# Kernel optimization log

Hardware: AMD Instinct MI355X
Metric: run time of the kernel (lower is better)

Reference implementation:

```python
import jax, jax.numpy as jnp
import numpy as np

# decoded layout constants
NN, NO, SD = 16, 8, 4          # num_neighbors, num_obstacles, state_dim_per_agent
B = 131072                      # batch rows
H1, E, HP, AD = 64, 16, 64, 2   # phi hidden, embed, psi hidden, action dim
D_ROBOT, D_OBST = 0.3, 0.3
B_GAMMA, B_EXPH = 0.05, 1.0
PHI_MIN, PHI_MAX = -2.0, 2.0
A_MAX = 2.0


def setup_inputs() -> dict:
    key = jax.random.key(0)
    kx, kw = jax.random.split(key)
    # x: [count | goal(SD) | NN neighbor rel-states (SD each) | NO obstacle rel-pos (2 each)]
    x = jax.random.normal(kx, (B, 1 + SD + SD * NN + 2 * NO), dtype=jnp.float32) * 2.0
    x = x.at[:, 0].set(float(NN))
    names = [("Wp1n", (SD, H1)), ("bp1n", (H1,)), ("Wp2n", (H1, E)), ("bp2n", (E,)),
             ("Wr1n", (E, H1)), ("br1n", (H1,)), ("Wr2n", (H1, E)), ("br2n", (E,)),
             ("Wp1o", (2, H1)), ("bp1o", (H1,)), ("Wp2o", (H1, E)), ("bp2o", (E,)),
             ("Wr1o", (E, H1)), ("br1o", (H1,)), ("Wr2o", (H1, E)), ("br2o", (E,)),
             ("Wpsi1", (2 * E + SD, HP)), ("bpsi1", (HP,)), ("Wpsi2", (HP, AD)), ("bpsi2", (AD,))]
    ks = jax.random.split(kw, len(names))
    inp = {"x": x}
    for (n, sh), k in zip(names, ks):
        s = 1.0 / np.sqrt(sh[0])  # torch Linear default init scale
        inp[n] = jax.random.uniform(k, sh, jnp.float32, -s, s)
    return inp


def _mlp2(h, W1, b1, W2, b2):
    # Feedforward: activation between layers, linear output
    return jax.nn.relu(h @ W1 + b1) @ W2 + b2


def _deepset(el, Wp1, bp1, Wp2, bp2, Wr1, br1, Wr2, br2):
    # el: [B, n, d] -> phi each element, sum over set, rho
    phi = _mlp2(el, Wp1, bp1, Wp2, bp2)          # [B, n, E]
    return _mlp2(phi.sum(axis=1), Wr1, br1, Wr2, br2)  # [B, E]


def _barrier_sum(P, D):
    # P: [B, n, 2]; APF barrier gamma * P / (|P| * (|P|-D)^exph), summed over n
    nrm = jnp.linalg.norm(P, axis=-1, keepdims=True)   # [B, n, 1]
    H = nrm - D
    return (B_GAMMA * P / (nrm * H ** B_EXPH)).sum(axis=1)  # [B, 2]


def reference(x, Wp1n, bp1n, Wp2n, bp2n, Wr1n, br1n, Wr2n, br2n,
              Wp1o, bp1o, Wp2o, bp2o, Wr1o, br1o, Wr2o, br2o,
              Wpsi1, bpsi1, Wpsi2, bpsi2):
    nb = x.shape[0]
    g = x[:, 1:1 + SD]                                        # goal
    nbr = x[:, 1 + SD:1 + SD + SD * NN].reshape(nb, NN, SD)   # neighbor rel-states
    obs = x[:, 1 + SD + SD * NN:].reshape(nb, NO, 2)          # obstacle rel-pos

    rho_n = _deepset(nbr, Wp1n, bp1n, Wp2n, bp2n, Wr1n, br1n, Wr2n, br2n)
    rho_o = _deepset(obs, Wp1o, bp1o, Wp2o, bp2o, Wr1o, br1o, Wr2o, br2o)

    h = jnp.concatenate([rho_n, rho_o, g], axis=1)            # [B, 2E+SD]
    emp = _mlp2(h, Wpsi1, bpsi1, Wpsi2, bpsi2)                # psi network
    emp = (jnp.tanh(emp) + 1.0) / 2.0 * (PHI_MAX - PHI_MIN) + PHI_MIN  # scale_empty

    bar = _barrier_sum(-nbr[:, :, :2], D_ROBOT) + _barrier_sum(-obs, D_OBST)

    action = emp + bar
    # scale(): divide rows whose inf-norm exceeds a_max
    inv_alpha = jnp.maximum(jnp.max(jnp.abs(action), axis=1, keepdims=True) / A_MAX, 1.0)
    return action / inv_alpha
```

## Files before the change

kernel.cpp:

```cpp
#include <hip/hip_runtime.h>
#include <math.h>


typedef __attribute__((ext_vector_type(8))) _Float16 f16x8;
typedef __attribute__((ext_vector_type(2))) __fp16 fp16x2;
typedef __attribute__((ext_vector_type(4))) float f32x4;

#define XW 85

#define FR_S1N  0
#define FR_S1O  4
#define FR_G2N  8
#define FR_G2O  10
#define FR_RNA  12
#define FR_RNB  16
#define FR_ROA  18
#define FR_ROB  22
#define FR_PSI1 24
#define FR_PSI2 32
#define N_FRAGS 34

#define BIG_STR 144
#define PHI_STR 80
#define CAT_STR 144
#define L_BIGN 0
#define L_BIGO 2304
#define L_PHN  4608
#define L_PHO  5888
#define L_CAT  7168
#define L_OUT  9472
#define L_BAR  9600
#define GRP_LDS 9728
#define NBA_STR 136
#define OBA_STR 68

#define H16_ONE 0x00003C00u

__device__ __forceinline__ float fast_rcp(float x)  { return __builtin_amdgcn_rcpf(x); }
__device__ __forceinline__ float fast_sqrt(float x) { return __builtin_amdgcn_sqrtf(x); }

__device__ __forceinline__ float two_tanh(float a) {
    float ax = fabsf(a);
    float e = __expf(2.0f * ax);
    float t = 1.0f - 2.0f * fast_rcp(e + 1.0f);
    return copysignf(2.0f * t, a);
}

__device__ __forceinline__ void lds_order() {
    __asm__ __volatile__("" ::: "memory");
}

__device__ __forceinline__ unsigned pk2(float a, float b) {
    union { fp16x2 h; unsigned u; } t;
    t.h = __builtin_amdgcn_cvt_pkrtz(a, b);
    return t.u;
}
__device__ __forceinline__ f16x8 lds_af(const char* area, int stride, int off, int lane) {
    int mm = lane & 15, qq = lane >> 4;
    return *(const f16x8*)(area + mm * stride + off + qq * 16);
}
__device__ __forceinline__ f16x8 load_bh(const _Float16* wsf, int frag, int lane) {
    return ((const f16x8*)(wsf + (size_t)frag * 512))[lane];
}
__device__ __forceinline__ f32x4 cinit(float b) {
    f32x4 c; c[0] = b; c[1] = b; c[2] = b; c[3] = b; return c;
}
__device__ __forceinline__ f32x4 mfma1(f16x8 a, f16x8 b, f32x4 c) {
    return __builtin_amdgcn_mfma_f32_16x16x32_f16(a, b, c, 0, 0, 0);
}

__global__ void bn_prep(const float* __restrict__ Wp1n, const float* __restrict__ Wp2n,
                        const float* __restrict__ Wr1n, const float* __restrict__ Wr2n,
                        const float* __restrict__ Wp1o, const float* __restrict__ Wp2o,
                        const float* __restrict__ Wr1o, const float* __restrict__ Wr2o,
                        const float* __restrict__ Wpsi1, const float* __restrict__ Wpsi2,
                        const float* __restrict__ bp1n, const float* __restrict__ bp1o,
                        const float* __restrict__ br1n, const float* __restrict__ br1o,
                        const float* __restrict__ bpsi1,
                        _Float16* __restrict__ wsf)
{
    int f = blockIdx.x;
    int lane = threadIdx.x;
    const float* W; const float* bias = nullptr;
    int K, N, kk = 0, nt = 0, rel, kbias = -1;
    if (f < 4)        { W = Wp1n;  K = 4;  N = 64; nt = f;      bias = bp1n;  kbias = 4; }
    else if (f < 8)   { W = Wp1o;  K = 2;  N = 64; nt = f - 4;  bias = bp1o;  kbias = 2; }
    else if (f < 10)  { W = Wp2n;  K = 64; N = 16; kk = f - 8; }
    else if (f < 12)  { W = Wp2o;  K = 64; N = 16; kk = f - 10; }
    else if (f < 16)  { W = Wr1n;  K = 16; N = 64; nt = f - 12; bias = br1n;  kbias = 16; }
    else if (f < 18)  { W = Wr2n;  K = 64; N = 16; kk = f - 16; }
    else if (f < 22)  { W = Wr1o;  K = 16; N = 64; nt = f - 18; bias = br1o;  kbias = 16; }
    else if (f < 24)  { W = Wr2o;  K = 64; N = 16; kk = f - 22; }
    else if (f < 32)  { rel = f - 24; W = Wpsi1; K = 36; N = 64; kk = rel >> 2; nt = rel & 3;
                        bias = bpsi1; kbias = 36; }
    else              { W = Wpsi2; K = 64; N = 2;  kk = f - 32; }

    int q = lane >> 4, c = lane & 15;
    _Float16* dst = wsf + (size_t)f * 512 + lane * 8;
    for (int j = 0; j < 8; ++j) {
        int k = kk * 32 + q * 8 + j;
        int n = nt * 16 + c;
        float v = 0.f;
        if (n < N) {
            if (k < K) v = W[k * N + n];
            else if (k == kbias) v = bias[n];
        }
        dst[j] = (_Float16)v;
    }
}

__global__ __launch_bounds__(256, 8) void bn_main(
    const float* __restrict__ x, const _Float16* __restrict__ wsf,
    const float* __restrict__ bp2n, const float* __restrict__ br2n,
    const float* __restrict__ bp2o, const float* __restrict__ br2o,
    const float* __restrict__ bpsi2,
    float* __restrict__ out, int nb)
{
    __shared__ char smem[2 * GRP_LDS];
    const int lane = threadIdx.x & 63;
    const int wid  = threadIdx.x >> 6;
    const int grp  = wid >> 1;
    const int role = wid & 1;
    const int group = blockIdx.x * 2 + grp;
    const int row0 = group * 16;

    char* Gl   = smem + grp * GRP_LDS;
    char* BIGN = Gl + L_BIGN;
    char* BIGO = Gl + L_BIGO;
    char* PHN  = Gl + L_PHN;
    char* PHO  = Gl + L_PHO;
    char* CAT  = Gl + L_CAT;
    char* OUTA = Gl + L_OUT;
    char* BAR  = Gl + L_BAR;
    char* NBA  = BIGN;
    char* OBA  = BIGO;

    const int m = lane & 15, q = lane >> 4, c = m;
    const float* xg   = x + (size_t)row0 * XW;
    const float* xrow = xg + (size_t)m * XW;

    const f32x4 ZC = cinit(0.f);

    if (role == 0) {
        {
            int ln5 = lane >> 5;
            int pr  = lane & 31;
            int mm0 = pr >> 1, fp = pr & 1;
            char* db = NBA + mm0 * NBA_STR + fp * 4;
            const float* s0 = xg + (size_t)ln5 * XW + 5 + pr * 2;
            #pragma unroll
            for (int t = 0; t < 8; ++t) {
                const float* s = s0 + (size_t)(2 * t) * XW;
                *(unsigned*)(db + (2 * t + ln5) * 8) = pk2(s[0], s[1]);
            }
        }

        {
            unsigned zv = ((lane & 7) == 0) ? H16_ONE : 0u;
            for (int i = lane; i < 128; i += 64) {
                int r = i >> 3, d = i & 7;
                *(unsigned*)(PHN + r * PHI_STR + 32 + d * 4) = zv;
            }
        }
        lds_order();

        f16x8 Bs1n[4];
        #pragma unroll
        for (int nt = 0; nt < 4; ++nt) Bs1n[nt] = load_bh(wsf, FR_S1N + nt, lane);

        {
            const int m8 = m * 8;
            f32x4 acc[4];
            #pragma unroll
            for (int nt = 0; nt < 4; ++nt) acc[nt] = cinit(0.f);
            union { f16x8 v; unsigned u[4]; uint2 h[2]; } A;
            A.u[2] = H16_ONE; A.u[3] = 0;
            #pragma unroll 8
            for (int mm = 0; mm < 16; ++mm) {
                A.h[0] = *(const uint2*)(NBA + mm * NBA_STR + m8);
                #pragma unroll
                for (int nt = 0; nt < 4; ++nt) {
                    f32x4 cc = mfma1(A.v, Bs1n[nt], ZC);
                    #pragma unroll
                    for (int reg = 0; reg < 4; ++reg)
                        acc[nt][reg] += fmaxf(cc[reg], 0.f);
                }
            }
            lds_order();
            #pragma unroll
            for (int nt = 0; nt < 4; ++nt)
                #pragma unroll
                for (int reg = 0; reg < 4; ++reg)
                    *(_Float16*)(BIGN + (q * 4 + reg) * BIG_STR + (nt * 16 + c) * 2)
                        = (_Float16)acc[nt][reg];
        }
        lds_order();

        {
            float b_g2n = 16.f * bp2n[c];
            f16x8 Bg2n0 = load_bh(wsf, FR_G2N + 0, lane);
            f16x8 Bg2n1 = load_bh(wsf, FR_G2N + 1, lane);
            f16x8 A0 = lds_af(BIGN, BIG_STR, 0, lane);
            f16x8 A1 = lds_af(BIGN, BIG_STR, 64, lane);
            f32x4 ca = mfma1(A0, Bg2n0, cinit(b_g2n));
            f32x4 cb = mfma1(A1, Bg2n1, ZC);
            #pragma unroll
            for (int reg = 0; reg < 4; ++reg)
                *(_Float16*)(PHN + (q * 4 + reg) * PHI_STR + c * 2) = (_Float16)(ca[reg] + cb[reg]);
        }
        lds_order();

        {
            f16x8 Brna[4];
            #pragma unroll
            for (int nt = 0; nt < 4; ++nt) Brna[nt] = load_bh(wsf, FR_RNA + nt, lane);
            f16x8 A = lds_af(PHN, PHI_STR, 0, lane);
            #pragma unroll
            for (int nt = 0; nt < 4; ++nt) {
                f32x4 cc = mfma1(A, Brna[nt], ZC);
                #pragma unroll
                for (int reg = 0; reg < 4; ++reg)
                    *(_Float16*)(BIGN + (q * 4 + reg) * BIG_STR + (nt * 16 + c) * 2) = (_Float16)fmaxf(cc[reg], 0.f);
            }
        }
        lds_order();

        {
            float b_rnb = br2n[c];
            f16x8 Brnb0 = load_bh(wsf, FR_RNB + 0, lane);
            f16x8 Brnb1 = load_bh(wsf, FR_RNB + 1, lane);
            f16x8 A0 = lds_af(BIGN, BIG_STR, 0, lane);
            f16x8 A1 = lds_af(BIGN, BIG_STR, 64, lane);
            f32x4 ca = mfma1(A0, Brnb0, cinit(b_rnb));
            f32x4 cb = mfma1(A1, Brnb1, ZC);
            #pragma unroll
            for (int reg = 0; reg < 4; ++reg)
                *(_Float16*)(CAT + (q * 4 + reg) * CAT_STR + c * 2) = (_Float16)(ca[reg] + cb[reg]);
        }
    } else {
        {
            int r8 = lane >> 3;
            int oo = lane & 7;
            char* db = OBA + oo * OBA_STR;
            const float* s0 = xg + (size_t)r8 * XW + 69 + oo * 2;
            #pragma unroll
            for (int t = 0; t < 2; ++t) {
                const float* s = s0 + (size_t)(8 * t) * XW;
                *(unsigned*)(db + (8 * t + r8) * 4) = pk2(s[0], s[1]);
            }
        }

        {
            unsigned zv = ((lane & 7) == 0) ? H16_ONE : 0u;
            for (int i = lane; i < 128; i += 64) {
                int r = i >> 3, d = i & 7;
                *(unsigned*)(PHO + r * PHI_STR + 32 + d * 4) = zv;
            }
        }
        {
            unsigned zc = ((lane & 15) == 2) ? H16_ONE : 0u;
            for (int i = lane; i < 256; i += 64) {
                int r = i >> 4, d = i & 15;
                *(unsigned*)(CAT + r * CAT_STR + 64 + d * 4) = zc;
            }
        }
        lds_order();

        if (lane < 16) {
            const float* xr = x + (size_t)(row0 + lane) * XW;
            uint2 gv;
            gv.x = pk2(xr[1], xr[2]);
            gv.y = pk2(xr[3], xr[4]);
            *(uint2*)(CAT + lane * CAT_STR + 64) = gv;
        }

        {
            float bx = 0.f, by = 0.f;
            #pragma unroll
            for (int i = 0; i < 4; ++i) {
                int n = 4 * q + i;
                float px = -xrow[5 + 4 * n], py = -xrow[6 + 4 * n];
                float nrm = fast_sqrt(px * px + py * py);
                float coef = 0.05f * fast_rcp(nrm * (nrm - 0.3f));
                bx = fmaf(coef, px, bx);
                by = fmaf(coef, py, by);
            }
            #pragma unroll
            for (int i = 0; i < 2; ++i) {
                int o = 2 * q + i;
                float px = -xrow[69 + 2 * o], py = -xrow[70 + 2 * o];
                float nrm = fast_sqrt(px * px + py * py);
                float coef = 0.05f * fast_rcp(nrm * (nrm - 0.3f));
                bx = fmaf(coef, px, bx);
                by = fmaf(coef, py, by);
            }
            bx += __shfl_xor(bx, 16); by += __shfl_xor(by, 16);
            bx += __shfl_xor(bx, 32); by += __shfl_xor(by, 32);
            if (q == 0) { float2 bb; bb.x = bx; bb.y = by; *(float2*)(BAR + m * 8) = bb; }
        }

        f16x8 Bs1o[4];
        #pragma unroll
        for (int nt = 0; nt < 4; ++nt) Bs1o[nt] = load_bh(wsf, FR_S1O + nt, lane);

        {
            const int m4 = m * 4;
            f32x4 acc[4];
            #pragma unroll
            for (int nt = 0; nt < 4; ++nt) acc[nt] = cinit(0.f);
            union { f16x8 v; unsigned u[4]; } A;
            A.u[1] = H16_ONE; A.u[2] = 0; A.u[3] = 0;
            #pragma unroll
            for (int oo = 0; oo < 8; ++oo) {
                A.u[0] = *(const unsigned*)(OBA + oo * OBA_STR + m4);
                #pragma unroll
                for (int nt = 0; nt < 4; ++nt) {
                    f32x4 cc = mfma1(A.v, Bs1o[nt], ZC);
                    #pragma unroll
                    for (int reg = 0; reg < 4; ++reg)
                        acc[nt][reg] += fmaxf(cc[reg], 0.f);
                }
            }
            lds_order();
            #pragma unroll
            for (int nt = 0; nt < 4; ++nt)
                #pragma unroll
                for (int reg = 0; reg < 4; ++reg)
                    *(_Float16*)(BIGO + (q * 4 + reg) * BIG_STR + (nt * 16 + c) * 2)
                        = (_Float16)acc[nt][reg];
        }
        lds_order();

        {
            float b_g2o = 8.f * bp2o[c];
            f16x8 Bg2o0 = load_bh(wsf, FR_G2O + 0, lane);
            f16x8 Bg2o1 = load_bh(wsf, FR_G2O + 1, lane);
            f16x8 A0 = lds_af(BIGO, BIG_STR, 0, lane);
            f16x8 A1 = lds_af(BIGO, BIG_STR, 64, lane);
            f32x4 ca = mfma1(A0, Bg2o0, cinit(b_g2o));
            f32x4 cb = mfma1(A1, Bg2o1, ZC);
            #pragma unroll
            for (int reg = 0; reg < 4; ++reg)
                *(_Float16*)(PHO + (q * 4 + reg) * PHI_STR + c * 2) = (_Float16)(ca[reg] + cb[reg]);
        }
        lds_order();

        {
            f16x8 Broa[4];
            #pragma unroll
            for (int nt = 0; nt < 4; ++nt) Broa[nt] = load_bh(wsf, FR_ROA + nt, lane);
            f16x8 A = lds_af(PHO, PHI_STR, 0, lane);
            #pragma unroll
            for (int nt = 0; nt < 4; ++nt) {
                f32x4 cc = mfma1(A, Broa[nt], ZC);
                #pragma unroll
                for (int reg = 0; reg < 4; ++reg)
                    *(_Float16*)(BIGO + (q * 4 + reg) * BIG_STR + (nt * 16 + c) * 2) = (_Float16)fmaxf(cc[reg], 0.f);
            }
        }
        lds_order();

        {
            float b_rob = br2o[c];
            f16x8 Brob0 = load_bh(wsf, FR_ROB + 0, lane);
            f16x8 Brob1 = load_bh(wsf, FR_ROB + 1, lane);
            f16x8 A0 = lds_af(BIGO, BIG_STR, 0, lane);
            f16x8 A1 = lds_af(BIGO, BIG_STR, 64, lane);
            f32x4 ca = mfma1(A0, Brob0, cinit(b_rob));
            f32x4 cb = mfma1(A1, Brob1, ZC);
            #pragma unroll
            for (int reg = 0; reg < 4; ++reg)
                *(_Float16*)(CAT + (q * 4 + reg) * CAT_STR + (16 + c) * 2) = (_Float16)(ca[reg] + cb[reg]);
        }
    }

    __syncthreads();

    if (role == 1) {
        f16x8 Bp1a[4], Bp1b[4], Bp2[2];
        #pragma unroll
        for (int nt = 0; nt < 4; ++nt) Bp1a[nt] = load_bh(wsf, FR_PSI1 + nt, lane);
        #pragma unroll
        for (int nt = 0; nt < 4; ++nt) Bp1b[nt] = load_bh(wsf, FR_PSI1 + 4 + nt, lane);
        Bp2[0] = load_bh(wsf, FR_PSI2 + 0, lane);
        Bp2[1] = load_bh(wsf, FR_PSI2 + 1, lane);

        {
            f16x8 A0 = lds_af(CAT, CAT_STR, 0, lane);
            f16x8 A1 = lds_af(CAT, CAT_STR, 64, lane);
            #pragma unroll
            for (int nt = 0; nt < 4; ++nt) {
                f32x4 ca = mfma1(A0, Bp1a[nt], ZC);
                f32x4 cb = mfma1(A1, Bp1b[nt], ZC);
                #pragma unroll
                for (int reg = 0; reg < 4; ++reg)
                    *(_Float16*)(BIGO + (q * 4 + reg) * BIG_STR + (nt * 16 + c) * 2) = (_Float16)fmaxf(ca[reg] + cb[reg], 0.f);
            }
        }
        lds_order();

        {
            float b_p2 = (c < 2) ? bpsi2[c] : 0.f;
            f16x8 A0 = lds_af(BIGO, BIG_STR, 0, lane);
            f16x8 A1 = lds_af(BIGO, BIG_STR, 64, lane);
            f32x4 ca = mfma1(A0, Bp2[0], cinit(b_p2));
            f32x4 cb = mfma1(A1, Bp2[1], ZC);
            if (c < 2) {
                #pragma unroll
                for (int reg = 0; reg < 4; ++reg)
                    *(float*)(OUTA + (q * 4 + reg) * 8 + c * 4) = ca[reg] + cb[reg];
            }
        }
        lds_order();

        if (lane < 16) {
            float2 a  = *(const float2*)(OUTA + lane * 8);
            float2 bb = *(const float2*)(BAR + lane * 8);
            float a0 = two_tanh(a.x) + bb.x;
            float a1 = two_tanh(a.y) + bb.y;
            float amax = fmaxf(fabsf(a0), fabsf(a1));
            float inv_alpha = fmaxf(amax * 0.5f, 1.0f);
            float rr = fast_rcp(inv_alpha);
            float2 o; o.x = a0 * rr; o.y = a1 * rr;
            *(float2*)(out + (size_t)(row0 + lane) * 2) = o;
        }
    }
}

extern "C" void kernel_launch(void* const* d_in, const int* in_sizes, int n_in,
                              void* d_out, int out_size, void* d_ws, size_t ws_size,
                              hipStream_t stream) {
    const float* x     = (const float*)d_in[0];
    const float* Wp1n  = (const float*)d_in[1];
    const float* bp1n  = (const float*)d_in[2];
    const float* Wp2n  = (const float*)d_in[3];
    const float* bp2n  = (const float*)d_in[4];
    const float* Wr1n  = (const float*)d_in[5];
    const float* br1n  = (const float*)d_in[6];
    const float* Wr2n  = (const float*)d_in[7];
    const float* br2n  = (const float*)d_in[8];
    const float* Wp1o  = (const float*)d_in[9];
    const float* bp1o  = (const float*)d_in[10];
    const float* Wp2o  = (const float*)d_in[11];
    const float* bp2o  = (const float*)d_in[12];
    const float* Wr1o  = (const float*)d_in[13];
    const float* br1o  = (const float*)d_in[14];
    const float* Wr2o  = (const float*)d_in[15];
    const float* br2o  = (const float*)d_in[16];
    const float* Wpsi1 = (const float*)d_in[17];
    const float* bpsi1 = (const float*)d_in[18];
    const float* Wpsi2 = (const float*)d_in[19];
    const float* bpsi2 = (const float*)d_in[20];
    float* out = (float*)d_out;

    int nb = in_sizes[0] / XW;
    _Float16* wsf = (_Float16*)d_ws;

    bn_prep<<<N_FRAGS, 64, 0, stream>>>(Wp1n, Wp2n, Wr1n, Wr2n,
                                        Wp1o, Wp2o, Wr1o, Wr2o,
                                        Wpsi1, Wpsi2,
                                        bp1n, bp1o, br1n, br1o, bpsi1,
                                        wsf);

    int groups = (nb + 15) / 16;
    int blocks = (groups + 1) / 2;
    bn_main<<<blocks, 256, 0, stream>>>(x, wsf,
                                        bp2n, br2n, bp2o, br2o, bpsi2,
                                        out, nb);
}
```

Before: 145.4 us.

## Process each 16-row group with one wavefront instead of two cooperating waves

Before, two waves shared each 16-row group: one ran the neighbor deep-set, the other the obstacle deep-set, barrier and psi, joined by a block-wide barrier. Now each wave handles a whole group serially with a smaller, reused per-wave LDS region, so a 256-thread block covers four groups and the __syncthreads disappears. The aim is to drop the cross-wave sync and shrink LDS per group. The cost is a longer serial dependency chain per wave and less overlap between the two branches. Launch bounds drop from 8 to 6 blocks per CU.

```diff
diff --git a/kernel.cpp b/kernel.cpp
--- a/kernel.cpp
+++ b/kernel.cpp
@@ -23,14 +23,13 @@
 #define BIG_STR 144
 #define PHI_STR 80
 #define CAT_STR 144
-#define L_BIGN 0
-#define L_BIGO 2304
-#define L_PHN  4608
-#define L_PHO  5888
-#define L_CAT  7168
-#define L_OUT  9472
-#define L_BAR  9600
-#define GRP_LDS 9728
+#define L_BIG  0
+#define L_PHI  2304
+#define L_CAT  3584
+#define L_OUT  5888
+#define L_BAR  6016
+#define L_OBA  6144
+#define GRP_LDS 6688
 #define NBA_STR 136
 #define OBA_STR 68
 
@@ -109,31 +108,27 @@
     }
 }
 
-__global__ __launch_bounds__(256, 8) void bn_main(
+__global__ __launch_bounds__(256, 6) void bn_main(
     const float* __restrict__ x, const _Float16* __restrict__ wsf,
     const float* __restrict__ bp2n, const float* __restrict__ br2n,
     const float* __restrict__ bp2o, const float* __restrict__ br2o,
     const float* __restrict__ bpsi2,
     float* __restrict__ out, int nb)
 {
-    __shared__ char smem[2 * GRP_LDS];
+    __shared__ char smem[4 * GRP_LDS];
     const int lane = threadIdx.x & 63;
     const int wid  = threadIdx.x >> 6;
-    const int grp  = wid >> 1;
-    const int role = wid & 1;
-    const int group = blockIdx.x * 2 + grp;
+    const int group = blockIdx.x * 4 + wid;
     const int row0 = group * 16;
 
-    char* Gl   = smem + grp * GRP_LDS;
-    char* BIGN = Gl + L_BIGN;
-    char* BIGO = Gl + L_BIGO;
-    char* PHN  = Gl + L_PHN;
-    char* PHO  = Gl + L_PHO;
+    char* Gl   = smem + wid * GRP_LDS;
+    char* BIG  = Gl + L_BIG;
+    char* PHI  = Gl + L_PHI;
     char* CAT  = Gl + L_CAT;
     char* OUTA = Gl + L_OUT;
     char* BAR  = Gl + L_BAR;
-    char* NBA  = BIGN;
-    char* OBA  = BIGO;
+    char* OBA  = Gl + L_OBA;
+    char* NBA  = BIG;
 
     const int m = lane & 15, q = lane >> 4, c = m;
     const float* xg   = x + (size_t)row0 * XW;
@@ -141,289 +136,273 @@
 
     const f32x4 ZC = cinit(0.f);
 
-    if (role == 0) {
-        {
-            int ln5 = lane >> 5;
-            int pr  = lane & 31;
-            int mm0 = pr >> 1, fp = pr & 1;
-            char* db = NBA + mm0 * NBA_STR + fp * 4;
-            const float* s0 = xg + (size_t)ln5 * XW + 5 + pr * 2;
-            #pragma unroll
-            for (int t = 0; t < 8; ++t) {
-                const float* s = s0 + (size_t)(2 * t) * XW;
-                *(unsigned*)(db + (2 * t + ln5) * 8) = pk2(s[0], s[1]);
-            }
-        }
-
-        {
-            unsigned zv = ((lane & 7) == 0) ? H16_ONE : 0u;
-            for (int i = lane; i < 128; i += 64) {
-                int r = i >> 3, d = i & 7;
-                *(unsigned*)(PHN + r * PHI_STR + 32 + d * 4) = zv;
-            }
-        }
-        lds_order();
-
+    {
+        int ln5 = lane >> 5;
+        int pr  = lane & 31;
+        int mm0 = pr >> 1, fp = pr & 1;
+        char* db = NBA + mm0 * NBA_STR + fp * 4;
+        const float* s0 = xg + (size_t)ln5 * XW + 5 + pr * 2;
+        #pragma unroll
+        for (int t = 0; t < 8; ++t) {
+            const float* s = s0 + (size_t)(2 * t) * XW;
+            *(unsigned*)(db + (2 * t + ln5) * 8) = pk2(s[0], s[1]);
+        }
+    }
+    {
+        int r8 = lane >> 3;
+        int oo = lane & 7;
+        char* db = OBA + oo * OBA_STR;
+        const float* s0 = xg + (size_t)r8 * XW + 69 + oo * 2;
+        #pragma unroll
+        for (int t = 0; t < 2; ++t) {
+            const float* s = s0 + (size_t)(8 * t) * XW;
+            *(unsigned*)(db + (8 * t + r8) * 4) = pk2(s[0], s[1]);
+        }
+    }
+
+    {
+        unsigned zv = ((lane & 7) == 0) ? H16_ONE : 0u;
+        for (int i = lane; i < 128; i += 64) {
+            int r = i >> 3, d = i & 7;
+            *(unsigned*)(PHI + r * PHI_STR + 32 + d * 4) = zv;
+        }
+    }
+    {
+        unsigned zc = ((lane & 15) == 2) ? H16_ONE : 0u;
+        for (int i = lane; i < 256; i += 64) {
+            int r = i >> 4, d = i & 15;
+            *(unsigned*)(CAT + r * CAT_STR + 64 + d * 4) = zc;
+        }
+    }
+    if (lane < 16) {
+        const float* xr = x + (size_t)(row0 + lane) * XW;
+        uint2 gv;
+        gv.x = pk2(xr[1], xr[2]);
+        gv.y = pk2(xr[3], xr[4]);
+        *(uint2*)(CAT + lane * CAT_STR + 64) = gv;
+    }
+
+    {
+        float bx = 0.f, by = 0.f;
+        #pragma unroll
+        for (int i = 0; i < 4; ++i) {
+            int n = 4 * q + i;
+            float px = -xrow[5 + 4 * n], py = -xrow[6 + 4 * n];
+            float nrm = fast_sqrt(px * px + py * py);
+            float coef = 0.05f * fast_rcp(nrm * (nrm - 0.3f));
+            bx = fmaf(coef, px, bx);
+            by = fmaf(coef, py, by);
+        }
+        #pragma unroll
+        for (int i = 0; i < 2; ++i) {
+            int o = 2 * q + i;
+            float px = -xrow[69 + 2 * o], py = -xrow[70 + 2 * o];
+            float nrm = fast_sqrt(px * px + py * py);
+            float coef = 0.05f * fast_rcp(nrm * (nrm - 0.3f));
+            bx = fmaf(coef, px, bx);
+            by = fmaf(coef, py, by);
+        }
+        bx += __shfl_xor(bx, 16); by += __shfl_xor(by, 16);
+        bx += __shfl_xor(bx, 32); by += __shfl_xor(by, 32);
+        if (q == 0) { float2 bb; bb.x = bx; bb.y = by; *(float2*)(BAR + m * 8) = bb; }
+    }
+    lds_order();
+
+    {
         f16x8 Bs1n[4];
         #pragma unroll
         for (int nt = 0; nt < 4; ++nt) Bs1n[nt] = load_bh(wsf, FR_S1N + nt, lane);
 
-        {
-            const int m8 = m * 8;
-            f32x4 acc[4];
-            #pragma unroll
-            for (int nt = 0; nt < 4; ++nt) acc[nt] = cinit(0.f);
-            union { f16x8 v; unsigned u[4]; uint2 h[2]; } A;
-            A.u[2] = H16_ONE; A.u[3] = 0;
-            #pragma unroll 8
-            for (int mm = 0; mm < 16; ++mm) {
-                A.h[0] = *(const uint2*)(NBA + mm * NBA_STR + m8);
-                #pragma unroll
-                for (int nt = 0; nt < 4; ++nt) {
-                    f32x4 cc = mfma1(A.v, Bs1n[nt], ZC);
-                    #pragma unroll
-                    for (int reg = 0; reg < 4; ++reg)
-                        acc[nt][reg] += fmaxf(cc[reg], 0.f);
-                }
-            }
-            lds_order();
-            #pragma unroll
-            for (int nt = 0; nt < 4; ++nt)
+        const int m8 = m * 8;
+        f32x4 acc[4];
+        #pragma unroll
+        for (int nt = 0; nt < 4; ++nt) acc[nt] = cinit(0.f);
+        union { f16x8 v; unsigned u[4]; uint2 h[2]; } A;
+        A.u[2] = H16_ONE; A.u[3] = 0;
+        #pragma unroll 8
+        for (int mm = 0; mm < 16; ++mm) {
+            A.h[0] = *(const uint2*)(NBA + mm * NBA_STR + m8);
+            #pragma unroll
+            for (int nt = 0; nt < 4; ++nt) {
+                f32x4 cc = mfma1(A.v, Bs1n[nt], ZC);
                 #pragma unroll
                 for (int reg = 0; reg < 4; ++reg)
-                    *(_Float16*)(BIGN + (q * 4 + reg) * BIG_STR + (nt * 16 + c) * 2)
-                        = (_Float16)acc[nt][reg];
+                    acc[nt][reg] += fmaxf(cc[reg], 0.f);
+            }
         }
         lds_order();
-
-        {
-            float b_g2n = 16.f * bp2n[c];
-            f16x8 Bg2n0 = load_bh(wsf, FR_G2N + 0, lane);
-            f16x8 Bg2n1 = load_bh(wsf, FR_G2N + 1, lane);
-            f16x8 A0 = lds_af(BIGN, BIG_STR, 0, lane);
-            f16x8 A1 = lds_af(BIGN, BIG_STR, 64, lane);
-            f32x4 ca = mfma1(A0, Bg2n0, cinit(b_g2n));
-            f32x4 cb = mfma1(A1, Bg2n1, ZC);
-            #pragma unroll
-            for (int reg = 0; reg < 4; ++reg)
-                *(_Float16*)(PHN + (q * 4 + reg) * PHI_STR + c * 2) = (_Float16)(ca[reg] + cb[reg]);
-        }
-        lds_order();
-
-        {
-            f16x8 Brna[4];
-            #pragma unroll
-            for (int nt = 0; nt < 4; ++nt) Brna[nt] = load_bh(wsf, FR_RNA + nt, lane);
-            f16x8 A = lds_af(PHN, PHI_STR, 0, lane);
+        #pragma unroll
+        for (int nt = 0; nt < 4; ++nt)
+            #pragma unroll
+            for (int reg = 0; reg < 4; ++reg)
+                *(_Float16*)(BIG + (q * 4 + reg) * BIG_STR + (nt * 16 + c) * 2)
+                    = (_Float16)acc[nt][reg];
+    }
+    lds_order();
+
+    {
+        float b_g2n = 16.f * bp2n[c];
+        f16x8 Bg2n0 = load_bh(wsf, FR_G2N + 0, lane);
+        f16x8 Bg2n1 = load_bh(wsf, FR_G2N + 1, lane);
+        f16x8 A0 = lds_af(BIG, BIG_STR, 0, lane);
+        f16x8 A1 = lds_af(BIG, BIG_STR, 64, lane);
+        f32x4 ca = mfma1(A0, Bg2n0, cinit(b_g2n));
+        f32x4 cb = mfma1(A1, Bg2n1, ZC);
+        #pragma unroll
+        for (int reg = 0; reg < 4; ++reg)
+            *(_Float16*)(PHI + (q * 4 + reg) * PHI_STR + c * 2) = (_Float16)(ca[reg] + cb[reg]);
+    }
+    lds_order();
+
+    {
+        f16x8 Brna[4];
+        #pragma unroll
+        for (int nt = 0; nt < 4; ++nt) Brna[nt] = load_bh(wsf, FR_RNA + nt, lane);
+        f16x8 A = lds_af(PHI, PHI_STR, 0, lane);
+        #pragma unroll
+        for (int nt = 0; nt < 4; ++nt) {
+            f32x4 cc = mfma1(A, Brna[nt], ZC);
+            #pragma unroll
+            for (int reg = 0; reg < 4; ++reg)
+                *(_Float16*)(BIG + (q * 4 + reg) * BIG_STR + (nt * 16 + c) * 2) = (_Float16)fmaxf(cc[reg], 0.f);
+        }
+    }
+    lds_order();
+
+    {
+        float b_rnb = br2n[c];
+        f16x8 Brnb0 = load_bh(wsf, FR_RNB + 0, lane);
+        f16x8 Brnb1 = load_bh(wsf, FR_RNB + 1, lane);
+        f16x8 A0 = lds_af(BIG, BIG_STR, 0, lane);
+        f16x8 A1 = lds_af(BIG, BIG_STR, 64, lane);
+        f32x4 ca = mfma1(A0, Brnb0, cinit(b_rnb));
+        f32x4 cb = mfma1(A1, Brnb1, ZC);
+        #pragma unroll
+        for (int reg = 0; reg < 4; ++reg)
+            *(_Float16*)(CAT + (q * 4 + reg) * CAT_STR + c * 2) = (_Float16)(ca[reg] + cb[reg]);
+    }
+    lds_order();
+
+    {
+        f16x8 Bs1o[4];
+        #pragma unroll
+        for (int nt = 0; nt < 4; ++nt) Bs1o[nt] = load_bh(wsf, FR_S1O + nt, lane);
+
+        const int m4 = m * 4;
+        f32x4 acc[4];
+        #pragma unroll
+        for (int nt = 0; nt < 4; ++nt) acc[nt] = cinit(0.f);
+        union { f16x8 v; unsigned u[4]; } A;
+        A.u[1] = H16_ONE; A.u[2] = 0; A.u[3] = 0;
+        #pragma unroll
+        for (int oo = 0; oo < 8; ++oo) {
+            A.u[0] = *(const unsigned*)(OBA + oo * OBA_STR + m4);
             #pragma unroll
             for (int nt = 0; nt < 4; ++nt) {
-                f32x4 cc = mfma1(A, Brna[nt], ZC);
+                f32x4 cc = mfma1(A.v, Bs1o[nt], ZC);
                 #pragma unroll
                 for (int reg = 0; reg < 4; ++reg)
-                    *(_Float16*)(BIGN + (q * 4 + reg) * BIG_STR + (nt * 16 + c) * 2) = (_Float16)fmaxf(cc[reg], 0.f);
+                    acc[nt][reg] += fmaxf(cc[reg], 0.f);
             }
         }
         lds_order();
-
-        {
-            float b_rnb = br2n[c];
-            f16x8 Brnb0 = load_bh(wsf, FR_RNB + 0, lane);
-            f16x8 Brnb1 = load_bh(wsf, FR_RNB + 1, lane);
-            f16x8 A0 = lds_af(BIGN, BIG_STR, 0, lane);
-            f16x8 A1 = lds_af(BIGN, BIG_STR, 64, lane);
-            f32x4 ca = mfma1(A0, Brnb0, cinit(b_rnb));
-            f32x4 cb = mfma1(A1, Brnb1, ZC);
-            #pragma unroll
-            for (int reg = 0; reg < 4; ++reg)
-                *(_Float16*)(CAT + (q * 4 + reg) * CAT_STR + c * 2) = (_Float16)(ca[reg] + cb[reg]);
-        }
-    } else {
-        {
-            int r8 = lane >> 3;
-            int oo = lane & 7;
-            char* db = OBA + oo * OBA_STR;
-            const float* s0 = xg + (size_t)r8 * XW + 69 + oo * 2;
-            #pragma unroll
-            for (int t = 0; t < 2; ++t) {
-                const float* s = s0 + (size_t)(8 * t) * XW;
-                *(unsigned*)(db + (8 * t + r8) * 4) = pk2(s[0], s[1]);
-            }
-        }
-
-        {
-            unsigned zv = ((lane & 7) == 0) ? H16_ONE : 0u;
-            for (int i = lane; i < 128; i += 64) {
-                int r = i >> 3, d = i & 7;
-                *(unsigned*)(PHO + r * PHI_STR + 32 + d * 4) = zv;
-            }
-        }
-        {
-            unsigned zc = ((lane & 15) == 2) ? H16_ONE : 0u;
-            for (int i = lane; i < 256; i += 64) {
-                int r = i >> 4, d = i & 15;
-                *(unsigned*)(CAT + r * CAT_STR + 64 + d * 4) = zc;
-            }
-        }
-        lds_order();
-
-        if (lane < 16) {
-            const float* xr = x + (size_t)(row0 + lane) * XW;
-            uint2 gv;
-            gv.x = pk2(xr[1], xr[2]);
-            gv.y = pk2(xr[3], xr[4]);
-            *(uint2*)(CAT + lane * CAT_STR + 64) = gv;
-        }
-
-        {
-            float bx = 0.f, by = 0.f;
-            #pragma unroll
-            for (int i = 0; i < 4; ++i) {
-                int n = 4 * q + i;
-                float px = -xrow[5 + 4 * n], py = -xrow[6 + 4 * n];
-                float nrm = fast_sqrt(px * px + py * py);
-                float coef = 0.05f * fast_rcp(nrm * (nrm - 0.3f));
-                bx = fmaf(coef, px, bx);
-                by = fmaf(coef, py, by);
-            }
-            #pragma unroll
-            for (int i = 0; i < 2; ++i) {
-                int o = 2 * q + i;
-                float px = -xrow[69 + 2 * o], py = -xrow[70 + 2 * o];
-                float nrm = fast_sqrt(px * px + py * py);
-                float coef = 0.05f * fast_rcp(nrm * (nrm - 0.3f));
-                bx = fmaf(coef, px, bx);
-                by = fmaf(coef, py, by);
-            }
-            bx += __shfl_xor(bx, 16); by += __shfl_xor(by, 16);
-            bx += __shfl_xor(bx, 32); by += __shfl_xor(by, 32);
-            if (q == 0) { float2 bb; bb.x = bx; bb.y = by; *(float2*)(BAR + m * 8) = bb; }
-        }
-
-        f16x8 Bs1o[4];
-        #pragma unroll
-        for (int nt = 0; nt < 4; ++nt) Bs1o[nt] = load_bh(wsf, FR_S1O + nt, lane);
-
-        {
-            const int m4 = m * 4;
-            f32x4 acc[4];
-            #pragma unroll
-            for (int nt = 0; nt < 4; ++nt) acc[nt] = cinit(0.f);
-            union { f16x8 v; unsigned u[4]; } A;
-            A.u[1] = H16_ONE; A.u[2] = 0; A.u[3] = 0;
-            #pragma unroll
-            for (int oo = 0; oo < 8; ++oo) {
-                A.u[0] = *(const unsigned*)(OBA + oo * OBA_STR + m4);
-                #pragma unroll
-                for (int nt = 0; nt < 4; ++nt) {
-                    f32x4 cc = mfma1(A.v, Bs1o[nt], ZC);
-                    #pragma unroll
-                    for (int reg = 0; reg < 4; ++reg)
-                        acc[nt][reg] += fmaxf(cc[reg], 0.f);
-                }
-            }
-            lds_order();
-            #pragma unroll
-            for (int nt = 0; nt < 4; ++nt)
-                #pragma unroll
-                for (int reg = 0; reg < 4; ++reg)
-                    *(_Float16*)(BIGO + (q * 4 + reg) * BIG_STR + (nt * 16 + c) * 2)
-                        = (_Float16)acc[nt][reg];
-        }
-        lds_order();
-
-        {
-            float b_g2o = 8.f * bp2o[c];
-            f16x8 Bg2o0 = load_bh(wsf, FR_G2O + 0, lane);
-            f16x8 Bg2o1 = load_bh(wsf, FR_G2O + 1, lane);
-            f16x8 A0 = lds_af(BIGO, BIG_STR, 0, lane);
-            f16x8 A1 = lds_af(BIGO, BIG_STR, 64, lane);
-            f32x4 ca = mfma1(A0, Bg2o0, cinit(b_g2o));
-            f32x4 cb = mfma1(A1, Bg2o1, ZC);
-            #pragma unroll
-            for (int reg = 0; reg < 4; ++reg)
-                *(_Float16*)(PHO + (q * 4 + reg) * PHI_STR + c * 2) = (_Float16)(ca[reg] + cb[reg]);
-        }
-        lds_order();
-
-        {
-            f16x8 Broa[4];
-            #pragma unroll
-            for (int nt = 0; nt < 4; ++nt) Broa[nt] = load_bh(wsf, FR_ROA + nt, lane);
-            f16x8 A = lds_af(PHO, PHI_STR, 0, lane);
-            #pragma unroll
-            for (int nt = 0; nt < 4; ++nt) {
-                f32x4 cc = mfma1(A, Broa[nt], ZC);
-                #pragma unroll
-                for (int reg = 0; reg < 4; ++reg)
-                    *(_Float16*)(BIGO + (q * 4 + reg) * BIG_STR + (nt * 16 + c) * 2) = (_Float16)fmaxf(cc[reg], 0.f);
-            }
-        }
-        lds_order();
-
-        {
-            float b_rob = br2o[c];
-            f16x8 Brob0 = load_bh(wsf, FR_ROB + 0, lane);
-            f16x8 Brob1 = load_bh(wsf, FR_ROB + 1, lane);
-            f16x8 A0 = lds_af(BIGO, BIG_STR, 0, lane);
-            f16x8 A1 = lds_af(BIGO, BIG_STR, 64, lane);
-            f32x4 ca = mfma1(A0, Brob0, cinit(b_rob));
-            f32x4 cb = mfma1(A1, Brob1, ZC);
-            #pragma unroll
-            for (int reg = 0; reg < 4; ++reg)
-                *(_Float16*)(CAT + (q * 4 + reg) * CAT_STR + (16 + c) * 2) = (_Float16)(ca[reg] + cb[reg]);
-        }
-    }
-
-    __syncthreads();
-
-    if (role == 1) {
-        f16x8 Bp1a[4], Bp1b[4], Bp2[2];
+        #pragma unroll
+        for (int nt = 0; nt < 4; ++nt)
+            #pragma unroll
+            for (int reg = 0; reg < 4; ++reg)
+                *(_Float16*)(BIG + (q * 4 + reg) * BIG_STR + (nt * 16 + c) * 2)
+                    = (_Float16)acc[nt][reg];
+    }
+    lds_order();
+
+    {
+        float b_g2o = 8.f * bp2o[c];
+        f16x8 Bg2o0 = load_bh(wsf, FR_G2O + 0, lane);
+        f16x8 Bg2o1 = load_bh(wsf, FR_G2O + 1, lane);
+        f16x8 A0 = lds_af(BIG, BIG_STR, 0, lane);
+        f16x8 A1 = lds_af(BIG, BIG_STR, 64, lane);
+        f32x4 ca = mfma1(A0, Bg2o0, cinit(b_g2o));
+        f32x4 cb = mfma1(A1, Bg2o1, ZC);
+        #pragma unroll
+        for (int reg = 0; reg < 4; ++reg)
+            *(_Float16*)(PHI + (q * 4 + reg) * PHI_STR + c * 2) = (_Float16)(ca[reg] + cb[reg]);
+    }
+    lds_order();
+
+    {
+        f16x8 Broa[4];
+        #pragma unroll
+        for (int nt = 0; nt < 4; ++nt) Broa[nt] = load_bh(wsf, FR_ROA + nt, lane);
+        f16x8 A = lds_af(PHI, PHI_STR, 0, lane);
+        #pragma unroll
+        for (int nt = 0; nt < 4; ++nt) {
+            f32x4 cc = mfma1(A, Broa[nt], ZC);
+            #pragma unroll
+            for (int reg = 0; reg < 4; ++reg)
+                *(_Float16*)(BIG + (q * 4 + reg) * BIG_STR + (nt * 16 + c) * 2) = (_Float16)fmaxf(cc[reg], 0.f);
+        }
+    }
+    lds_order();
+
+    {
+        float b_rob = br2o[c];
+        f16x8 Brob0 = load_bh(wsf, FR_ROB + 0, lane);
+        f16x8 Brob1 = load_bh(wsf, FR_ROB + 1, lane);
+        f16x8 A0 = lds_af(BIG, BIG_STR, 0, lane);
+        f16x8 A1 = lds_af(BIG, BIG_STR, 64, lane);
+        f32x4 ca = mfma1(A0, Brob0, cinit(b_rob));
+        f32x4 cb = mfma1(A1, Brob1, ZC);
+        #pragma unroll
+        for (int reg = 0; reg < 4; ++reg)
+            *(_Float16*)(CAT + (q * 4 + reg) * CAT_STR + (16 + c) * 2) = (_Float16)(ca[reg] + cb[reg]);
+    }
+    lds_order();
+
+    {
+        f16x8 Bp1a[4], Bp1b[4];
         #pragma unroll
         for (int nt = 0; nt < 4; ++nt) Bp1a[nt] = load_bh(wsf, FR_PSI1 + nt, lane);
         #pragma unroll
         for (int nt = 0; nt < 4; ++nt) Bp1b[nt] = load_bh(wsf, FR_PSI1 + 4 + nt, lane);
-        Bp2[0] = load_bh(wsf, FR_PSI2 + 0, lane);
-        Bp2[1] = load_bh(wsf, FR_PSI2 + 1, lane);
-
-        {
-            f16x8 A0 = lds_af(CAT, CAT_STR, 0, lane);
-            f16x8 A1 = lds_af(CAT, CAT_STR, 64, lane);
-            #pragma unroll
-            for (int nt = 0; nt < 4; ++nt) {
-                f32x4 ca = mfma1(A0, Bp1a[nt], ZC);
-                f32x4 cb = mfma1(A1, Bp1b[nt], ZC);
-                #pragma unroll
-                for (int reg = 0; reg < 4; ++reg)
-                    *(_Float16*)(BIGO + (q * 4 + reg) * BIG_STR + (nt * 16 + c) * 2) = (_Float16)fmaxf(ca[reg] + cb[reg], 0.f);
-            }
-        }
-        lds_order();
-
-        {
-            float b_p2 = (c < 2) ? bpsi2[c] : 0.f;
-            f16x8 A0 = lds_af(BIGO, BIG_STR, 0, lane);
-            f16x8 A1 = lds_af(BIGO, BIG_STR, 64, lane);
-            f32x4 ca = mfma1(A0, Bp2[0], cinit(b_p2));
-            f32x4 cb = mfma1(A1, Bp2[1], ZC);
-            if (c < 2) {
-                #pragma unroll
-                for (int reg = 0; reg < 4; ++reg)
-                    *(float*)(OUTA + (q * 4 + reg) * 8 + c * 4) = ca[reg] + cb[reg];
-            }
-        }
-        lds_order();
-
-        if (lane < 16) {
-            float2 a  = *(const float2*)(OUTA + lane * 8);
-            float2 bb = *(const float2*)(BAR + lane * 8);
-            float a0 = two_tanh(a.x) + bb.x;
-            float a1 = two_tanh(a.y) + bb.y;
-            float amax = fmaxf(fabsf(a0), fabsf(a1));
-            float inv_alpha = fmaxf(amax * 0.5f, 1.0f);
-            float rr = fast_rcp(inv_alpha);
-            float2 o; o.x = a0 * rr; o.y = a1 * rr;
-            *(float2*)(out + (size_t)(row0 + lane) * 2) = o;
-        }
+        f16x8 A0 = lds_af(CAT, CAT_STR, 0, lane);
+        f16x8 A1 = lds_af(CAT, CAT_STR, 64, lane);
+        #pragma unroll
+        for (int nt = 0; nt < 4; ++nt) {
+            f32x4 ca = mfma1(A0, Bp1a[nt], ZC);
+            f32x4 cb = mfma1(A1, Bp1b[nt], ZC);
+            #pragma unroll
+            for (int reg = 0; reg < 4; ++reg)
+                *(_Float16*)(BIG + (q * 4 + reg) * BIG_STR + (nt * 16 + c) * 2) = (_Float16)fmaxf(ca[reg] + cb[reg], 0.f);
+        }
+    }
+    lds_order();
+
+    {
+        float b_p2 = (c < 2) ? bpsi2[c] : 0.f;
+        f16x8 Bp20 = load_bh(wsf, FR_PSI2 + 0, lane);
+        f16x8 Bp21 = load_bh(wsf, FR_PSI2 + 1, lane);
+        f16x8 A0 = lds_af(BIG, BIG_STR, 0, lane);
+        f16x8 A1 = lds_af(BIG, BIG_STR, 64, lane);
+        f32x4 ca = mfma1(A0, Bp20, cinit(b_p2));
+        f32x4 cb = mfma1(A1, Bp21, ZC);
+        if (c < 2) {
+            #pragma unroll
+            for (int reg = 0; reg < 4; ++reg)
+                *(float*)(OUTA + (q * 4 + reg) * 8 + c * 4) = ca[reg] + cb[reg];
+        }
+    }
+    lds_order();
+
+    if (lane < 16) {
+        float2 a  = *(const float2*)(OUTA + lane * 8);
+        float2 bb = *(const float2*)(BAR + lane * 8);
+        float a0 = two_tanh(a.x) + bb.x;
+        float a1 = two_tanh(a.y) + bb.y;
+        float amax = fmaxf(fabsf(a0), fabsf(a1));
+        float inv_alpha = fmaxf(amax * 0.5f, 1.0f);
+        float rr = fast_rcp(inv_alpha);
+        float2 o; o.x = a0 * rr; o.y = a1 * rr;
+        *(float2*)(out + (size_t)(row0 + lane) * 2) = o;
     }
 }
 
@@ -463,7 +442,7 @@
                                         wsf);
 
     int groups = (nb + 15) / 16;
-    int blocks = (groups + 1) / 2;
+    int blocks = (groups + 3) / 4;
     bn_main<<<blocks, 256, 0, stream>>>(x, wsf,
                                         bp2n, br2n, bp2o, br2o, bpsi2,
                                         out, nb);
```

Measured after the change: 145.3 us. About the same (-0.1%).
